# Kernel tuning notes

Measured on AMD Instinct MI355X. Metric: run time of the kernel, lower is better.

Reference implementation:

```python
import jax, jax.numpy as jnp
import numpy as np

N = 100_000      # nodes
E = 1_600_000    # edges (avg degree 16)
IN_DIM = 256
HID = 128
N_OUT = 2


def _linear_params(key, fan_in, fan_out):
    kw, kb = jax.random.split(key)
    bound = 1.0 / np.sqrt(fan_in)
    W = jax.random.uniform(kw, (fan_in, fan_out), jnp.float32, -bound, bound)
    b = jax.random.uniform(kb, (fan_out,), jnp.float32, -bound, bound)
    return W, b


def setup_inputs() -> dict:
    key = jax.random.key(0)
    ks = jax.random.split(key, 6)
    edge_index = jax.random.randint(ks[0], (2, E), 0, N, dtype=jnp.int64)
    x = jax.random.normal(ks[1], (N, IN_DIM), jnp.float32)
    Wi, bi = _linear_params(ks[2], IN_DIM, HID)   # NodeInitializer.lin
    W1, b1 = _linear_params(ks[3], HID, HID)      # GCNConv 1
    W2, b2 = _linear_params(ks[4], HID, HID)      # GCNConv 2
    Wh, bh = _linear_params(ks[5], HID, N_OUT)    # head
    return {"edge_index": edge_index, "x": x, "Wi": Wi, "bi": bi,
            "W1": W1, "b1": b1, "W2": W2, "b2": b2, "Wh": Wh, "bh": bh}


def reference(edge_index, x, Wi, bi, W1, b1, W2, b2, Wh, bh):
    n = x.shape[0]
    # GCNConv preprocessing: add self-loops, symmetric degree normalization.
    loops = jnp.arange(n, dtype=edge_index.dtype)
    src = jnp.concatenate([edge_index[0], loops])  # message source
    dst = jnp.concatenate([edge_index[1], loops])  # aggregation target
    deg = jax.ops.segment_sum(jnp.ones(src.shape[0], jnp.float32), dst, num_segments=n)
    dinv = jnp.where(deg > 0, deg ** -0.5, 0.0)
    norm = dinv[src] * dinv[dst]                   # [E+N]

    # NodeInitializer: relu(linear(x)); dropout = identity (eval mode)
    h = jax.nn.relu(x @ Wi + bi)

    # Two GCNConv layers (no relu between, matching SimpleGCN.forward)
    for W, b in ((W1, b1), (W2, b2)):
        msg = (h @ W)[src] * norm[:, None]         # gather + normalize, [E+N, HID]
        h = jax.ops.segment_sum(msg, dst, num_segments=n) + b  # scatter-add

    return h @ Wh + bh                             # [N, N_OUT]
```

## Files before the change

### kernel.cpp

```cpp
#include <hip/hip_runtime.h>
#include <hip/hip_bf16.h>

#define N_NODES 100000
#define N_EDGES 1600000
#define DIM_IN  256
#define DIM_H   128

#define NBKT 782
#define CPAD 16
#define CAP  4096
#define EPB  8192
#define NBLK ((N_EDGES + EPB - 1) / EPB)

typedef __attribute__((ext_vector_type(8))) short short8;
typedef __attribute__((ext_vector_type(4))) float f32x4;

__device__ __forceinline__ int get_src(const int* e, int is64, int i) {
  return is64 ? e[2 * i] : e[i];
}
__device__ __forceinline__ int get_dst(const int* e, int is64, int i) {
  return is64 ? e[2 * (N_EDGES + i)] : e[N_EDGES + i];
}

__device__ __forceinline__ ushort f2bf(float f) {
  unsigned u = __float_as_uint(f);
  unsigned r = (u + 0x7fffu + ((u >> 16) & 1u)) >> 16;
  return (ushort)r;
}
__device__ __forceinline__ float bf2f(ushort h) {
  return __uint_as_float(((unsigned)h) << 16);
}

__device__ __forceinline__ void load8(const float* p, float* o) {
  float4 a = reinterpret_cast<const float4*>(p)[0];
  float4 b = reinterpret_cast<const float4*>(p)[1];
  o[0] = a.x; o[1] = a.y; o[2] = a.z; o[3] = a.w;
  o[4] = b.x; o[5] = b.y; o[6] = b.z; o[7] = b.w;
}

__device__ __forceinline__ void cvt_split(const float* v, short8& h, short8& l) {
#pragma unroll
  for (int j = 0; j < 8; ++j) {
    ushort hb = f2bf(v[j]);
    ushort lb = f2bf(v[j] - bf2f(hb));
    h[j] = (short)hb;
    l[j] = (short)lb;
  }
}

__global__ __launch_bounds__(256)
void k_prep(const float* __restrict__ Wi, const float* __restrict__ W1,
            const float* __restrict__ W2, const float* __restrict__ Wh,
            const float* __restrict__ b1, const float* __restrict__ b2,
            const float* __restrict__ bh, ushort* __restrict__ outHi,
            float* __restrict__ Wcc, int* __restrict__ bcnt) {
  __shared__ float Wc2s[DIM_H][2];
  constexpr int CH = DIM_IN / 32;
  if (blockIdx.x == 17) {
    for (int i = threadIdx.x; i < NBKT * CPAD; i += 256) bcnt[i] = 0;
    return;
  }
  if (blockIdx.x == 16) {
    const int t = threadIdx.x;
    const int i = t >> 1, j = t & 1;
    float s = 0.f;
#pragma unroll 4
    for (int m = 0; m < DIM_H; ++m) s += W2[(size_t)i * DIM_H + m] * Wh[m * 2 + j];
    Wc2s[i][j] = s;
    __syncthreads();
    float c = 0.f;
#pragma unroll 4
    for (int k = 0; k < DIM_H; ++k) c += W1[(size_t)i * DIM_H + k] * Wc2s[k][j];
    Wcc[i * 2 + j] = c;
    if (t < 2) {
      float a = 0.f, b = 0.f;
      for (int k = 0; k < DIM_H; ++k) {
        a += b1[k] * Wc2s[k][t];
        b += b2[k] * Wh[k * 2 + t];
      }
      Wcc[256 + t] = a;
      Wcc[258 + t] = b + bh[t];
    }
    return;
  }
  int idx = blockIdx.x * 256 + threadIdx.x;
  int n  = idx & 15;
  int qq = (idx >> 4) & 3;
  int nt = (idx >> 6) & 7;
  int c  = idx >> 9;
  int col = nt * 16 + n;
  short8 h8, l8;
#pragma unroll
  for (int j = 0; j < 8; ++j) {
    float v = Wi[(size_t)(c * 32 + qq * 8 + j) * DIM_H + col];
    ushort hb = f2bf(v);
    ushort lb = f2bf(v - bf2f(hb));
    h8[j] = (short)hb;
    l8[j] = (short)lb;
  }
  ((short8*)outHi)[idx] = h8;
  ((short8*)outHi)[CH * 512 + idx] = l8;
}

__global__ __launch_bounds__(1024)
void k_bin1(const int* __restrict__ eidx, int* __restrict__ bcnt,
            unsigned* __restrict__ ebuf) {
  __shared__ int hist[NBKT];
  __shared__ int curL[NBKT];
  __shared__ int s_or;
  const int t = threadIdx.x;
  if (t == 0) s_or = 0;
  for (int i = t; i < NBKT; i += 1024) hist[i] = 0;
  __syncthreads();
  if (eidx[2 * t + 1] != 0) atomicOr(&s_or, 1);
  __syncthreads();
  const int is64 = (s_or == 0);

  unsigned rec[EPB / 1024];
  int bkt[EPB / 1024];
#pragma unroll
  for (int j = 0; j < EPB / 1024; ++j) {
    int e = blockIdx.x * EPB + j * 1024 + t;
    bkt[j] = -1;
    rec[j] = 0;
    if (e < N_EDGES) {
      unsigned s = (unsigned)get_src(eidx, is64, e);
      unsigned d = (unsigned)get_dst(eidx, is64, e);
      if (s < N_NODES && d < N_NODES) {
        bkt[j] = (int)(d >> 7);
        rec[j] = s | ((d & 127u) << 17);
        atomicAdd(&hist[bkt[j]], 1);
      }
    }
  }
  __syncthreads();
  for (int i = t; i < NBKT; i += 1024) {
    int h = hist[i];
    curL[i] = h ? atomicAdd(&bcnt[i * CPAD], h) : 0;
  }
  __syncthreads();
#pragma unroll
  for (int j = 0; j < EPB / 1024; ++j) {
    if (bkt[j] >= 0) {
      int pos = atomicAdd(&curL[bkt[j]], 1);
      ebuf[(size_t)bkt[j] * CAP + pos] = rec[j];
    }
  }
}

__global__ __launch_bounds__(256)
void k_dinvB(const int* __restrict__ bcnt, const unsigned* __restrict__ ebuf,
             float* __restrict__ dinv) {
  __shared__ int hist[128];
  const int b = blockIdx.x, t = threadIdx.x;
  if (t < 128) hist[t] = 0;
  __syncthreads();
  const int cnt = bcnt[b * CPAD];
  const unsigned* eb = ebuf + (size_t)b * CAP;
  for (int i = t; i < cnt; i += 256) atomicAdd(&hist[eb[i] >> 17], 1);
  __syncthreads();
  if (t < 128) {
    int node = (b << 7) + t;
    if (node < N_NODES) dinv[node] = rsqrtf(1.0f + (float)hist[t]);
  }
}

template <int K>
__global__ __launch_bounds__(256, 4)
void k_gemm_xz(const float* __restrict__ A, const ushort* __restrict__ Bfrag,
               const float* __restrict__ bias, const float* __restrict__ Wcc,
               const float* __restrict__ dinv, float4* __restrict__ tbl) {
  constexpr int CH = K / 32;
  __shared__ __align__(16) ushort AhiS[2][256 * 8];
  __shared__ __align__(16) ushort AloS[2][256 * 8];
  const int tid = threadIdx.x;
  const int m0 = blockIdx.x * 64;
  const int wave = tid >> 6, lane = tid & 63;
  const int m_l = lane & 15, quad = lane >> 4;
  const int rs = tid >> 2, q = tid & 3;

  f32x4 acc[2][4];
#pragma unroll
  for (int i = 0; i < 2; ++i)
#pragma unroll
    for (int j = 0; j < 4; ++j) acc[i][j] = (f32x4){0.f, 0.f, 0.f, 0.f};

  const short8* Bhi8 = (const short8*)Bfrag;
  const short8* Blo8 = Bhi8 + CH * 512;
  short8* Ah = (short8*)AhiS;
  short8* Al = (short8*)AloS;

  const int gr = m0 + rs;
  const float* Ap = &A[(size_t)((gr < N_NODES) ? gr : (N_NODES - 1)) * K + q * 8];
  const int went = (rs >> 4) * 64 + q * 16 + ((rs & 15) ^ (q << 2));
  const int rent = quad * 16 + (m_l ^ (quad << 2));

  {
    float v[8];
    load8(Ap, v);
    short8 h, l;
    cvt_split(v, h, l);
    Ah[went] = h;
    Al[went] = l;
  }
  const int bq = quad * 16 + m_l;
  short8 bh0 = Bhi8[(wave * 2 + 0) * 64 + bq];
  short8 bl0 = Blo8[(wave * 2 + 0) * 64 + bq];
  short8 bh1 = Bhi8[(wave * 2 + 1) * 64 + bq];
  short8 bl1 = Blo8[(wave * 2 + 1) * 64 + bq];
  __syncthreads();

#pragma unroll
  for (int c = 0; c < CH; ++c) {
    const int cur = c & 1, nxt = cur ^ 1;
    float vn[8];
    short8 nbh0, nbl0, nbh1, nbl1;
    if (c + 1 < CH) {
      load8(Ap + (c + 1) * 32, vn);
      const int b0 = ((c + 1) * 8 + wave * 2 + 0) * 64 + bq;
      const int b1 = ((c + 1) * 8 + wave * 2 + 1) * 64 + bq;
      nbh0 = Bhi8[b0]; nbl0 = Blo8[b0];
      nbh1 = Bhi8[b1]; nbl1 = Blo8[b1];
    }
    const short8* AhC = Ah + cur * 256;
    const short8* AlC = Al + cur * 256;
#pragma unroll
    for (int mt = 0; mt < 4; ++mt) {
      short8 ahi = AhC[mt * 64 + rent];
      short8 alo = AlC[mt * 64 + rent];
      acc[0][mt] = __builtin_amdgcn_mfma_f32_16x16x32_bf16(ahi, bh0, acc[0][mt], 0, 0, 0);
      acc[0][mt] = __builtin_amdgcn_mfma_f32_16x16x32_bf16(ahi, bl0, acc[0][mt], 0, 0, 0);
      acc[0][mt] = __builtin_amdgcn_mfma_f32_16x16x32_bf16(alo, bh0, acc[0][mt], 0, 0, 0);
      acc[1][mt] = __builtin_amdgcn_mfma_f32_16x16x32_bf16(ahi, bh1, acc[1][mt], 0, 0, 0);
      acc[1][mt] = __builtin_amdgcn_mfma_f32_16x16x32_bf16(ahi, bl1, acc[1][mt], 0, 0, 0);
      acc[1][mt] = __builtin_amdgcn_mfma_f32_16x16x32_bf16(alo, bh1, acc[1][mt], 0, 0, 0);
    }
    if (c + 1 < CH) {
      short8 h, l;
      cvt_split(vn, h, l);
      Ah[nxt * 256 + went] = h;
      Al[nxt * 256 + went] = l;
      bh0 = nbh0; bl0 = nbl0; bh1 = nbh1; bl1 = nbl1;
    }
    __syncthreads();
  }

  float p0[4][4], p1[4][4];
#pragma unroll
  for (int mt = 0; mt < 4; ++mt)
#pragma unroll
    for (int r = 0; r < 4; ++r) { p0[mt][r] = 0.f; p1[mt][r] = 0.f; }
#pragma unroll
  for (int ntl = 0; ntl < 2; ++ntl) {
    const int colg = (wave * 2 + ntl) * 16 + m_l;
    const float bv = bias[colg];
    const float w0 = Wcc[colg * 2 + 0];
    const float w1 = Wcc[colg * 2 + 1];
#pragma unroll
    for (int mt = 0; mt < 4; ++mt)
#pragma unroll
      for (int r = 0; r < 4; ++r) {
        float hv = fmaxf(acc[ntl][mt][r] + bv, 0.f);
        p0[mt][r] += hv * w0;
        p1[mt][r] += hv * w1;
      }
  }
#pragma unroll
  for (int o = 1; o < 16; o <<= 1) {
#pragma unroll
    for (int mt = 0; mt < 4; ++mt)
#pragma unroll
      for (int r = 0; r < 4; ++r) {
        p0[mt][r] += __shfl_xor(p0[mt][r], o);
        p1[mt][r] += __shfl_xor(p1[mt][r], o);
      }
  }
  float* zred = (float*)AhiS;
  if (m_l == 0) {
#pragma unroll
    for (int mt = 0; mt < 4; ++mt)
#pragma unroll
      for (int r = 0; r < 4; ++r) {
        zred[(((0 * 4 + wave) * 4 + quad) * 4 + mt) * 4 + r] = p0[mt][r];
        zred[(((1 * 4 + wave) * 4 + quad) * 4 + mt) * 4 + r] = p1[mt][r];
      }
  }
  __syncthreads();
  if (tid < 64) {
    const int mt = tid >> 4, qd = (tid >> 2) & 3, r = tid & 3;
    const int rowg = m0 + tid;
    if (rowg < N_NODES) {
      float s0 = 0.f, s1 = 0.f;
#pragma unroll
      for (int w = 0; w < 4; ++w) {
        s0 += zred[(((0 * 4 + w) * 4 + qd) * 4 + mt) * 4 + r];
        s1 += zred[(((1 * 4 + w) * 4 + qd) * 4 + mt) * 4 + r];
      }
      float dn = dinv[rowg];
      tbl[rowg] = make_float4(dn * s0, dn * s1, dn, 0.f);
    }
  }
}

__global__ __launch_bounds__(256)
void k_aggr1B(const int* __restrict__ bcnt, const unsigned* __restrict__ ebuf,
              const float4* __restrict__ tbl, float2* __restrict__ tb2,
              float* __restrict__ g) {
  __shared__ float acc[128][4];
  const int b = blockIdx.x, t = threadIdx.x;
  if (t < 128) { acc[t][0] = 0.f; acc[t][1] = 0.f; acc[t][2] = 0.f; }
  __syncthreads();
  const int cnt = bcnt[b * CPAD];
  const unsigned* eb = ebuf + (size_t)b * CAP;
  for (int i = t; i < cnt; i += 256) {
    unsigned r = eb[i];
    float4 v = tbl[r & 0x1FFFFu];
    int d = r >> 17;
    atomicAdd(&acc[d][0], v.x);
    atomicAdd(&acc[d][1], v.y);
    atomicAdd(&acc[d][2], v.z);
  }
  __syncthreads();
  if (t < 128) {
    int node = (b << 7) + t;
    if (node < N_NODES) {
      float4 self = tbl[node];
      float dn = self.z;
      tb2[node] = make_float2(dn * dn * (acc[t][0] + self.x),
                              dn * dn * (acc[t][1] + self.y));
      g[node] = dn * (acc[t][2] + self.z);
    }
  }
}

__global__ __launch_bounds__(256)
void k_aggr2B(const int* __restrict__ bcnt, const unsigned* __restrict__ ebuf,
              const float2* __restrict__ tb2, const float4* __restrict__ tbl,
              const float* __restrict__ g, const float* __restrict__ tail,
              float* __restrict__ out) {
  __shared__ float acc[128][2];
  const int b = blockIdx.x, t = threadIdx.x;
  if (t < 128) { acc[t][0] = 0.f; acc[t][1] = 0.f; }
  __syncthreads();
  const int cnt = bcnt[b * CPAD];
  const unsigned* eb = ebuf + (size_t)b * CAP;
  for (int i = t; i < cnt; i += 256) {
    unsigned r = eb[i];
    float2 v = tb2[r & 0x1FFFFu];
    int d = r >> 17;
    atomicAdd(&acc[d][0], v.x);
    atomicAdd(&acc[d][1], v.y);
  }
  __syncthreads();
  if (t < 128) {
    int node = (b << 7) + t;
    if (node < N_NODES) {
      float2 self = tb2[node];
      float dn = tbl[node].z;
      float gv = g[node];
      float o0 = dn * (acc[t][0] + self.x) + gv * tail[0] + tail[2];
      float o1 = dn * (acc[t][1] + self.y) + gv * tail[1] + tail[3];
      reinterpret_cast<float2*>(out)[node] = make_float2(o0, o1);
    }
  }
}

__global__ __launch_bounds__(1024) void k_detect(const int* __restrict__ e,
                                                 int* __restrict__ flag) {
  __shared__ int s;
  if (threadIdx.x == 0) s = 0;
  __syncthreads();
  atomicOr(&s, e[2 * threadIdx.x + 1]);
  __syncthreads();
  if (threadIdx.x == 0) *flag = (s == 0) ? 1 : 0;
}

__global__ __launch_bounds__(256) void k_zero(int* __restrict__ p, int n) {
  int i = blockIdx.x * 256 + threadIdx.x;
  if (i < n) p[i] = 0;
}

__global__ __launch_bounds__(256) void k_count(const int* __restrict__ eidx,
                                               const int* __restrict__ flag,
                                               int* __restrict__ off) {
  int e = blockIdx.x * 256 + threadIdx.x;
  int is64 = *flag;
  if (e < N_EDGES) {
    unsigned d = (unsigned)get_dst(eidx, is64, e);
    if (d < N_NODES) atomicAdd(&off[d], 1);
  }
}

__global__ __launch_bounds__(256) void k_dinv_old(const int* __restrict__ off,
                                                  float* __restrict__ dinv) {
  int i = blockIdx.x * 256 + threadIdx.x;
  if (i < N_NODES) dinv[i] = rsqrtf(1.0f + (float)off[i]);
}

template <int K>
__global__ __launch_bounds__(256)
void k_gemm(const float* __restrict__ A, const float* __restrict__ B,
            const float* __restrict__ bias, const float* __restrict__ scale,
            float* __restrict__ C, const int do_relu) {
  __shared__ float As[64][33];
  const int tid = threadIdx.x;
  const int tx = tid & 15;
  const int ty = tid >> 4;
  const int m0 = blockIdx.x * 64;

  float acc[4][8];
#pragma unroll
  for (int i = 0; i < 4; ++i)
#pragma unroll
    for (int j = 0; j < 8; ++j) acc[i][j] = 0.f;

  const int rs = tid >> 2;
  const int ks = (tid & 3) * 8;

  for (int k0 = 0; k0 < K; k0 += 32) {
    float av8[8];
    const int gm = m0 + rs;
    if (gm < N_NODES) {
      load8(&A[(size_t)gm * K + k0 + ks], av8);
    } else {
#pragma unroll
      for (int j = 0; j < 8; ++j) av8[j] = 0.f;
    }
    __syncthreads();
#pragma unroll
    for (int j = 0; j < 8; ++j) As[rs][ks + j] = av8[j];
    __syncthreads();

    const float* Bp = B + (size_t)k0 * DIM_H + tx * 8;
#pragma unroll 4
    for (int k = 0; k < 32; ++k) {
      float bv[8];
      load8(Bp + (size_t)k * DIM_H, bv);
      float av[4];
#pragma unroll
      for (int rr = 0; rr < 4; ++rr) av[rr] = As[ty * 4 + rr][k];
#pragma unroll
      for (int rr = 0; rr < 4; ++rr)
#pragma unroll
        for (int cc = 0; cc < 8; ++cc)
          acc[rr][cc] = fmaf(av[rr], bv[cc], acc[rr][cc]);
    }
  }

  float bs[8];
  if (bias) {
    load8(bias + tx * 8, bs);
  } else {
#pragma unroll
    for (int j = 0; j < 8; ++j) bs[j] = 0.f;
  }
#pragma unroll
  for (int rr = 0; rr < 4; ++rr) {
    const int gm = m0 + ty * 4 + rr;
    if (gm < N_NODES) {
      float sc = scale ? scale[gm] : 1.0f;
      float v[8];
#pragma unroll
      for (int cc = 0; cc < 8; ++cc) {
        float t = acc[rr][cc] + bs[cc];
        if (do_relu) t = fmaxf(t, 0.f);
        v[cc] = t * sc;
      }
      float* Cp = &C[(size_t)gm * DIM_H + tx * 8];
      reinterpret_cast<float4*>(Cp)[0] = make_float4(v[0], v[1], v[2], v[3]);
      reinterpret_cast<float4*>(Cp)[1] = make_float4(v[4], v[5], v[6], v[7]);
    }
  }
}

__global__ __launch_bounds__(256)
void k_aggr_init(const float* __restrict__ t, const float* __restrict__ dinv,
                 const float* __restrict__ bias, float* __restrict__ h) {
  int idx = blockIdx.x * 256 + threadIdx.x;
  if (idx < N_NODES * DIM_H) {
    int i = idx >> 7;
    int c = idx & 127;
    float d = dinv[i];
    h[idx] = bias[c] + t[idx] * d * d;
  }
}

__global__ __launch_bounds__(256)
void k_aggr_edges(const int* __restrict__ eidx, const int* __restrict__ flag,
                  const float* __restrict__ t, const float* __restrict__ dinv,
                  float* __restrict__ h) {
  int e = blockIdx.x * 2 + (threadIdx.x >> 7);
  int c = threadIdx.x & 127;
  int is64 = *flag;
  if (e < N_EDGES) {
    unsigned s = (unsigned)get_src(eidx, is64, e);
    unsigned d = (unsigned)get_dst(eidx, is64, e);
    if (s < N_NODES && d < N_NODES) {
      float nrm = dinv[s] * dinv[d];
      unsafeAtomicAdd(&h[(size_t)d * DIM_H + c], t[(size_t)s * DIM_H + c] * nrm);
    }
  }
}

__global__ __launch_bounds__(256)
void k_head_f32(const float* __restrict__ h, const float* __restrict__ Wh,
                const float* __restrict__ bh, float* __restrict__ out) {
  int node = blockIdx.x * 4 + (threadIdx.x >> 6);
  int lane = threadIdx.x & 63;
  if (node >= N_NODES) return;
  float h0 = h[(size_t)node * DIM_H + lane];
  float h1 = h[(size_t)node * DIM_H + 64 + lane];
  float s0 = h0 * Wh[lane * 2 + 0] + h1 * Wh[(lane + 64) * 2 + 0];
  float s1 = h0 * Wh[lane * 2 + 1] + h1 * Wh[(lane + 64) * 2 + 1];
#pragma unroll
  for (int off = 32; off > 0; off >>= 1) {
    s0 += __shfl_down(s0, off);
    s1 += __shfl_down(s1, off);
  }
  if (lane == 0) {
    reinterpret_cast<float2*>(out)[node] = make_float2(s0 + bh[0], s1 + bh[1]);
  }
}

extern "C" void kernel_launch(void* const* d_in, const int* in_sizes, int n_in,
                              void* d_out, int out_size, void* d_ws, size_t ws_size,
                              hipStream_t stream) {
  (void)in_sizes; (void)n_in; (void)out_size;
  const int* eidx = (const int*)d_in[0];
  const float* x  = (const float*)d_in[1];
  const float* Wi = (const float*)d_in[2];
  const float* bi = (const float*)d_in[3];
  const float* W1 = (const float*)d_in[4];
  const float* b1 = (const float*)d_in[5];
  const float* W2 = (const float*)d_in[6];
  const float* b2 = (const float*)d_in[7];
  const float* Wh = (const float*)d_in[8];
  const float* bh = (const float*)d_in[9];
  float* out = (float*)d_out;

  const int gE  = (N_EDGES + 255) / 256;
  const int gM  = (N_NODES + 63) / 64;
  const int gW  = (N_NODES + 3) / 4;

  char* ws = (char*)d_ws;

  const size_t need1 = 16201600;

  if (ws_size >= need1) {
    float*    Wcc  = (float*)(ws + 4096);
    ushort*   bfWi = (ushort*)(ws + 8192);
    int*      bcnt = (int*)(ws + 139264);
    float*    dinv = (float*)(ws + 189312);
    float4*   tbl  = (float4*)(ws + 589312);
    float2*   tb2  = (float2*)(ws + 2189312);
    float*    g    = (float*)(ws + 2989312);
    unsigned* ebuf = (unsigned*)(ws + 3389312);

    k_prep<<<18, 256, 0, stream>>>(Wi, W1, W2, Wh, b1, b2, bh, bfWi, Wcc, bcnt);
    k_bin1<<<NBLK, 1024, 0, stream>>>(eidx, bcnt, ebuf);
    k_dinvB<<<NBKT, 256, 0, stream>>>(bcnt, ebuf, dinv);
    k_gemm_xz<DIM_IN><<<gM, 256, 0, stream>>>(x, bfWi, bi, Wcc, dinv, tbl);
    k_aggr1B<<<NBKT, 256, 0, stream>>>(bcnt, ebuf, tbl, tb2, g);
    k_aggr2B<<<NBKT, 256, 0, stream>>>(bcnt, ebuf, tb2, tbl, g, Wcc + 256, out);
  } else {
    const int gN  = (N_NODES + 255) / 256;
    int*   flag = (int*)ws;
    int*   off  = (int*)(ws + 4096);
    float* dinv = (float*)(ws + 404480);
    float* fbA  = (float*)(ws + 804864);
    float* fbB  = (float*)(ws + 804864 + (size_t)N_NODES * DIM_H * 4);
    const int gNH = (N_NODES * DIM_H + 255) / 256;
    const int gE2 = (N_EDGES + 1) / 2;
    k_detect<<<1, 1024, 0, stream>>>(eidx, flag);
    k_zero<<<gN, 256, 0, stream>>>(off, N_NODES);
    k_count<<<gE, 256, 0, stream>>>(eidx, flag, off);
    k_dinv_old<<<gN, 256, 0, stream>>>(off, dinv);

    k_gemm<DIM_IN><<<gM, 256, 0, stream>>>(x, Wi, bi, nullptr, fbA, 1);
    k_gemm<DIM_H><<<gM, 256, 0, stream>>>(fbA, W1, nullptr, nullptr, fbB, 0);
    k_aggr_init<<<gNH, 256, 0, stream>>>(fbB, dinv, b1, fbA);
    k_aggr_edges<<<gE2, 256, 0, stream>>>(eidx, flag, fbB, dinv, fbA);
    k_gemm<DIM_H><<<gM, 256, 0, stream>>>(fbA, W2, nullptr, nullptr, fbB, 0);
    k_aggr_init<<<gNH, 256, 0, stream>>>(fbB, dinv, b2, fbA);
    k_aggr_edges<<<gE2, 256, 0, stream>>>(eidx, flag, fbB, dinv, fbA);
    k_head_f32<<<gW, 256, 0, stream>>>(fbA, Wh, bh, out);
  }
}
```

Baseline: 291.2 us.

## Stage whole A tile in LDS upfront and reduce epilogue via padded LDS

The GEMM kernel now loads the entire 64xK fp32 A tile at the start with contiguous coalesced loads. It converts the tile to bf16 hi/lo and stores it in LDS, replacing the per-chunk double-buffered loads and per-chunk barriers. The epilogue's shuffle-based 16-lane reduction is replaced by writes to a padded LDS array that 64 threads sum serially. LDS use grows (about 64KB for K=256), so launch bounds drop to 2 blocks per CU, and the serial 64-term reduction on one wave may cost time.

```diff
diff --git a/kernel.cpp b/kernel.cpp
--- a/kernel.cpp
+++ b/kernel.cpp
@@ -166,42 +166,38 @@
 }
 
 template <int K>
-__global__ __launch_bounds__(256, 4)
+__global__ __launch_bounds__(256, 2)
 void k_gemm_xz(const float* __restrict__ A, const ushort* __restrict__ Bfrag,
                const float* __restrict__ bias, const float* __restrict__ Wcc,
                const float* __restrict__ dinv, float4* __restrict__ tbl) {
   constexpr int CH = K / 32;
-  __shared__ __align__(16) ushort AhiS[2][256 * 8];
-  __shared__ __align__(16) ushort AloS[2][256 * 8];
+  __shared__ __align__(16) ushort AS[2 * CH * 256 * 8];
   const int tid = threadIdx.x;
   const int m0 = blockIdx.x * 64;
   const int wave = tid >> 6, lane = tid & 63;
   const int m_l = lane & 15, quad = lane >> 4;
-  const int rs = tid >> 2, q = tid & 3;
-
-  f32x4 acc[2][4];
-#pragma unroll
-  for (int i = 0; i < 2; ++i)
-#pragma unroll
-    for (int j = 0; j < 4; ++j) acc[i][j] = (f32x4){0.f, 0.f, 0.f, 0.f};
 
   const short8* Bhi8 = (const short8*)Bfrag;
   const short8* Blo8 = Bhi8 + CH * 512;
-  short8* Ah = (short8*)AhiS;
-  short8* Al = (short8*)AloS;
-
-  const int gr = m0 + rs;
-  const float* Ap = &A[(size_t)((gr < N_NODES) ? gr : (N_NODES - 1)) * K + q * 8];
-  const int went = (rs >> 4) * 64 + q * 16 + ((rs & 15) ^ (q << 2));
-  const int rent = quad * 16 + (m_l ^ (quad << 2));
-
-  {
+  short8* A8 = (short8*)AS;
+
+  const size_t xlim = (size_t)N_NODES * K * 4 - 32;
+  const size_t gbase = (size_t)m0 * K * 4;
+#pragma unroll
+  for (int rr = 0; rr < 8; ++rr) {
+    const size_t off = (size_t)rr * 8192 + (size_t)tid * 32;
+    size_t ga = gbase + off;
+    if (ga > xlim) ga = xlim;
     float v[8];
-    load8(Ap, v);
+    load8((const float*)((const char*)A + ga), v);
     short8 h, l;
     cvt_split(v, h, l);
-    Ah[went] = h;
-    Al[went] = l;
+    const int row = (int)(off >> 10);
+    const int byr = (int)(off & 1023);
+    const int c = byr >> 7, q = (byr >> 5) & 3;
+    const int ent = c * 256 + (row >> 4) * 64 + q * 16 + ((row & 15) ^ (q << 2));
+    A8[ent] = h;
+    A8[2048 + ent] = l;
   }
   const int bq = quad * 16 + m_l;
   short8 bh0 = Bhi8[(wave * 2 + 0) * 64 + bq];
@@ -210,20 +206,24 @@
   short8 bl1 = Blo8[(wave * 2 + 1) * 64 + bq];
   __syncthreads();
 
+  f32x4 acc[2][4];
+#pragma unroll
+  for (int i = 0; i < 2; ++i)
+#pragma unroll
+    for (int j = 0; j < 4; ++j) acc[i][j] = (f32x4){0.f, 0.f, 0.f, 0.f};
+
+  const int rent = quad * 16 + (m_l ^ (quad << 2));
 #pragma unroll
   for (int c = 0; c < CH; ++c) {
-    const int cur = c & 1, nxt = cur ^ 1;
-    float vn[8];
     short8 nbh0, nbl0, nbh1, nbl1;
     if (c + 1 < CH) {
-      load8(Ap + (c + 1) * 32, vn);
       const int b0 = ((c + 1) * 8 + wave * 2 + 0) * 64 + bq;
       const int b1 = ((c + 1) * 8 + wave * 2 + 1) * 64 + bq;
       nbh0 = Bhi8[b0]; nbl0 = Blo8[b0];
       nbh1 = Bhi8[b1]; nbl1 = Blo8[b1];
     }
-    const short8* AhC = Ah + cur * 256;
-    const short8* AlC = Al + cur * 256;
+    const short8* AhC = A8 + c * 256;
+    const short8* AlC = A8 + 2048 + c * 256;
 #pragma unroll
     for (int mt = 0; mt < 4; ++mt) {
       short8 ahi = AhC[mt * 64 + rent];
@@ -236,13 +236,8 @@
       acc[1][mt] = __builtin_amdgcn_mfma_f32_16x16x32_bf16(alo, bh1, acc[1][mt], 0, 0, 0);
     }
     if (c + 1 < CH) {
-      short8 h, l;
-      cvt_split(vn, h, l);
-      Ah[nxt * 256 + went] = h;
-      Al[nxt * 256 + went] = l;
       bh0 = nbh0; bl0 = nbl0; bh1 = nbh1; bl1 = nbl1;
     }
-    __syncthreads();
   }
 
   float p0[4][4], p1[4][4];
@@ -265,37 +260,34 @@
         p1[mt][r] += hv * w1;
       }
   }
-#pragma unroll
-  for (int o = 1; o < 16; o <<= 1) {
+  __syncthreads();
+  float* zs = (float*)AS;
+  {
+    const int base = ((wave * 4 + quad) * 16 + m_l) * 33;
 #pragma unroll
     for (int mt = 0; mt < 4; ++mt)
 #pragma unroll
       for (int r = 0; r < 4; ++r) {
-        p0[mt][r] += __shfl_xor(p0[mt][r], o);
-        p1[mt][r] += __shfl_xor(p1[mt][r], o);
+        zs[base + mt * 4 + r]      = p0[mt][r];
+        zs[base + 16 + mt * 4 + r] = p1[mt][r];
       }
   }
-  float* zred = (float*)AhiS;
-  if (m_l == 0) {
-#pragma unroll
-    for (int mt = 0; mt < 4; ++mt)
-#pragma unroll
-      for (int r = 0; r < 4; ++r) {
-        zred[(((0 * 4 + wave) * 4 + quad) * 4 + mt) * 4 + r] = p0[mt][r];
-        zred[(((1 * 4 + wave) * 4 + quad) * 4 + mt) * 4 + r] = p1[mt][r];
+  __syncthreads();
+  if (tid < 64) {
+    const int row = tid;
+    const int mt = row >> 4, qd = (row >> 2) & 3, r = row & 3;
+    float s0 = 0.f, s1 = 0.f;
+#pragma unroll
+    for (int w = 0; w < 4; ++w) {
+      const int wb = (w * 4 + qd) * 16 * 33;
+#pragma unroll
+      for (int ml = 0; ml < 16; ++ml) {
+        s0 += zs[wb + ml * 33 + mt * 4 + r];
+        s1 += zs[wb + ml * 33 + 16 + mt * 4 + r];
       }
-  }
-  __syncthreads();
-  if (tid < 64) {
-    const int mt = tid >> 4, qd = (tid >> 2) & 3, r = tid & 3;
-    const int rowg = m0 + tid;
+    }
+    const int rowg = m0 + row;
     if (rowg < N_NODES) {
-      float s0 = 0.f, s1 = 0.f;
-#pragma unroll
-      for (int w = 0; w < 4; ++w) {
-        s0 += zred[(((0 * 4 + w) * 4 + qd) * 4 + mt) * 4 + r];
-        s1 += zred[(((1 * 4 + w) * 4 + qd) * 4 + mt) * 4 + r];
-      }
       float dn = dinv[rowg];
       tbl[rowg] = make_float4(dn * s0, dn * s1, dn, 0.f);
     }
```

Result: no change. 292.3 us (+0.4%).

## Fuse edge binning with input GEMM in one launch and compute degree via global atomics

Applied to the files above, without the earlier changes.

Merges the edge-bucketing kernel and the feature GEMM into a single heterogeneous launch, where the first blocks bin edges and the rest run the GEMM. The goal is to let the memory-bound binning overlap with the compute-heavy GEMM and to drop a launch boundary. Degrees are now counted with global atomics during binning instead of in a separate histogram pass, and a small scale kernel afterwards applies dinv. This adds contention from per-edge global atomics, an extra ztmp round trip, and binning blocks shrunk to 256 threads.

```diff
diff --git a/kernel.cpp b/kernel.cpp
--- a/kernel.cpp
+++ b/kernel.cpp
@@ -9,8 +9,9 @@
 #define NBKT 782
 #define CPAD 16
 #define CAP  4096
-#define EPB  8192
-#define NBLK ((N_EDGES + EPB - 1) / EPB)
+#define EPB2 4096
+#define NBLK2 ((N_EDGES + EPB2 - 1) / EPB2)
+#define GEMM_BLKS ((N_NODES + 63) / 64)
 
 typedef __attribute__((ext_vector_type(8))) short short8;
 typedef __attribute__((ext_vector_type(4))) float f32x4;
@@ -53,9 +54,15 @@
             const float* __restrict__ W2, const float* __restrict__ Wh,
             const float* __restrict__ b1, const float* __restrict__ b2,
             const float* __restrict__ bh, ushort* __restrict__ outHi,
-            float* __restrict__ Wcc, int* __restrict__ bcnt) {
+            float* __restrict__ Wcc, int* __restrict__ bcnt,
+            int* __restrict__ deg) {
   __shared__ float Wc2s[DIM_H][2];
   constexpr int CH = DIM_IN / 32;
+  if (blockIdx.x >= 18) {
+    int i = (blockIdx.x - 18) * 256 + threadIdx.x;
+    if (i < N_NODES) deg[i] = 0;
+    return;
+  }
   if (blockIdx.x == 17) {
     for (int i = threadIdx.x; i < NBKT * CPAD; i += 256) bcnt[i] = 0;
     return;
@@ -102,79 +109,62 @@
   ((short8*)outHi)[CH * 512 + idx] = l8;
 }
 
-__global__ __launch_bounds__(1024)
-void k_bin1(const int* __restrict__ eidx, int* __restrict__ bcnt,
-            unsigned* __restrict__ ebuf) {
-  __shared__ int hist[NBKT];
-  __shared__ int curL[NBKT];
-  __shared__ int s_or;
-  const int t = threadIdx.x;
-  if (t == 0) s_or = 0;
-  for (int i = t; i < NBKT; i += 1024) hist[i] = 0;
-  __syncthreads();
-  if (eidx[2 * t + 1] != 0) atomicOr(&s_or, 1);
-  __syncthreads();
-  const int is64 = (s_or == 0);
-
-  unsigned rec[EPB / 1024];
-  int bkt[EPB / 1024];
-#pragma unroll
-  for (int j = 0; j < EPB / 1024; ++j) {
-    int e = blockIdx.x * EPB + j * 1024 + t;
-    bkt[j] = -1;
-    rec[j] = 0;
-    if (e < N_EDGES) {
-      unsigned s = (unsigned)get_src(eidx, is64, e);
-      unsigned d = (unsigned)get_dst(eidx, is64, e);
-      if (s < N_NODES && d < N_NODES) {
-        bkt[j] = (int)(d >> 7);
-        rec[j] = s | ((d & 127u) << 17);
-        atomicAdd(&hist[bkt[j]], 1);
-      }
-    }
-  }
-  __syncthreads();
-  for (int i = t; i < NBKT; i += 1024) {
-    int h = hist[i];
-    curL[i] = h ? atomicAdd(&bcnt[i * CPAD], h) : 0;
-  }
-  __syncthreads();
-#pragma unroll
-  for (int j = 0; j < EPB / 1024; ++j) {
-    if (bkt[j] >= 0) {
-      int pos = atomicAdd(&curL[bkt[j]], 1);
-      ebuf[(size_t)bkt[j] * CAP + pos] = rec[j];
-    }
-  }
-}
-
-__global__ __launch_bounds__(256)
-void k_dinvB(const int* __restrict__ bcnt, const unsigned* __restrict__ ebuf,
-             float* __restrict__ dinv) {
-  __shared__ int hist[128];
-  const int b = blockIdx.x, t = threadIdx.x;
-  if (t < 128) hist[t] = 0;
-  __syncthreads();
-  const int cnt = bcnt[b * CPAD];
-  const unsigned* eb = ebuf + (size_t)b * CAP;
-  for (int i = t; i < cnt; i += 256) atomicAdd(&hist[eb[i] >> 17], 1);
-  __syncthreads();
-  if (t < 128) {
-    int node = (b << 7) + t;
-    if (node < N_NODES) dinv[node] = rsqrtf(1.0f + (float)hist[t]);
-  }
-}
-
-template <int K>
 __global__ __launch_bounds__(256, 4)
-void k_gemm_xz(const float* __restrict__ A, const ushort* __restrict__ Bfrag,
-               const float* __restrict__ bias, const float* __restrict__ Wcc,
-               const float* __restrict__ dinv, float4* __restrict__ tbl) {
-  constexpr int CH = K / 32;
-  __shared__ __align__(16) ushort AhiS[2][256 * 8];
-  __shared__ __align__(16) ushort AloS[2][256 * 8];
+void k_main(const int* __restrict__ eidx, const float* __restrict__ A,
+            const ushort* __restrict__ Bfrag, const float* __restrict__ bias,
+            const float* __restrict__ Wcc, int* __restrict__ bcnt,
+            unsigned* __restrict__ ebuf, int* __restrict__ deg,
+            float2* __restrict__ ztmp) {
+  __shared__ __align__(16) char smem[16384];
   const int tid = threadIdx.x;
-  const int m0 = blockIdx.x * 64;
+
+  if (blockIdx.x < NBLK2) {
+    int* hist = (int*)smem;
+    int* curL = hist + NBKT;
+    int* sorp = curL + NBKT;
+    if (tid == 0) *sorp = 0;
+    for (int i = tid; i < NBKT; i += 256) hist[i] = 0;
+    __syncthreads();
+    if (eidx[2 * tid + 1] != 0) atomicOr(sorp, 1);
+    __syncthreads();
+    const int is64 = (*sorp == 0);
+
+    unsigned rec[16];
+    int bkt[16];
+#pragma unroll
+    for (int j = 0; j < 16; ++j) {
+      int e = blockIdx.x * EPB2 + j * 256 + tid;
+      bkt[j] = -1;
+      rec[j] = 0;
+      if (e < N_EDGES) {
+        unsigned s = (unsigned)get_src(eidx, is64, e);
+        unsigned d = (unsigned)get_dst(eidx, is64, e);
+        if (s < N_NODES && d < N_NODES) {
+          bkt[j] = (int)(d >> 7);
+          rec[j] = s | ((d & 127u) << 17);
+          atomicAdd(&hist[bkt[j]], 1);
+          atomicAdd(&deg[d], 1);
+        }
+      }
+    }
+    __syncthreads();
+    for (int i = tid; i < NBKT; i += 256) {
+      int h = hist[i];
+      curL[i] = h ? atomicAdd(&bcnt[i * CPAD], h) : 0;
+    }
+    __syncthreads();
+#pragma unroll
+    for (int j = 0; j < 16; ++j) {
+      if (bkt[j] >= 0) {
+        int pos = atomicAdd(&curL[bkt[j]], 1);
+        ebuf[(size_t)bkt[j] * CAP + pos] = rec[j];
+      }
+    }
+    return;
+  }
+
+  constexpr int CH = DIM_IN / 32;
+  const int m0 = (blockIdx.x - NBLK2) * 64;
   const int wave = tid >> 6, lane = tid & 63;
   const int m_l = lane & 15, quad = lane >> 4;
   const int rs = tid >> 2, q = tid & 3;
@@ -187,11 +177,11 @@
 
   const short8* Bhi8 = (const short8*)Bfrag;
   const short8* Blo8 = Bhi8 + CH * 512;
-  short8* Ah = (short8*)AhiS;
-  short8* Al = (short8*)AloS;
+  short8* Ah = (short8*)smem;
+  short8* Al = (short8*)(smem + 8192);
 
   const int gr = m0 + rs;
-  const float* Ap = &A[(size_t)((gr < N_NODES) ? gr : (N_NODES - 1)) * K + q * 8];
+  const float* Ap = &A[(size_t)((gr < N_NODES) ? gr : (N_NODES - 1)) * DIM_IN + q * 8];
   const int went = (rs >> 4) * 64 + q * 16 + ((rs & 15) ^ (q << 2));
   const int rent = quad * 16 + (m_l ^ (quad << 2));
 
@@ -275,7 +265,7 @@
         p1[mt][r] += __shfl_xor(p1[mt][r], o);
       }
   }
-  float* zred = (float*)AhiS;
+  float* zred = (float*)smem;
   if (m_l == 0) {
 #pragma unroll
     for (int mt = 0; mt < 4; ++mt)
@@ -296,9 +286,19 @@
         s0 += zred[(((0 * 4 + w) * 4 + qd) * 4 + mt) * 4 + r];
         s1 += zred[(((1 * 4 + w) * 4 + qd) * 4 + mt) * 4 + r];
       }
-      float dn = dinv[rowg];
-      tbl[rowg] = make_float4(dn * s0, dn * s1, dn, 0.f);
-    }
+      ztmp[rowg] = make_float2(s0, s1);
+    }
+  }
+}
+
+__global__ __launch_bounds__(256)
+void k_scale(const int* __restrict__ deg, const float2* __restrict__ ztmp,
+             float4* __restrict__ tbl) {
+  int n = blockIdx.x * 256 + threadIdx.x;
+  if (n < N_NODES) {
+    float dn = rsqrtf(1.0f + (float)deg[n]);
+    float2 z = ztmp[n];
+    tbl[n] = make_float4(dn * z.x, dn * z.y, dn, 0.f);
   }
 }
 
@@ -541,25 +541,28 @@
   const int gE  = (N_EDGES + 255) / 256;
   const int gM  = (N_NODES + 63) / 64;
   const int gW  = (N_NODES + 3) / 4;
+  const int gN256 = (N_NODES + 255) / 256;
 
   char* ws = (char*)d_ws;
 
-  const size_t need1 = 16201600;
+  const size_t need1 = 17001600;
 
   if (ws_size >= need1) {
     float*    Wcc  = (float*)(ws + 4096);
     ushort*   bfWi = (ushort*)(ws + 8192);
     int*      bcnt = (int*)(ws + 139264);
-    float*    dinv = (float*)(ws + 189312);
-    float4*   tbl  = (float4*)(ws + 589312);
-    float2*   tb2  = (float2*)(ws + 2189312);
-    float*    g    = (float*)(ws + 2989312);
-    unsigned* ebuf = (unsigned*)(ws + 3389312);
-
-    k_prep<<<18, 256, 0, stream>>>(Wi, W1, W2, Wh, b1, b2, bh, bfWi, Wcc, bcnt);
-    k_bin1<<<NBLK, 1024, 0, stream>>>(eidx, bcnt, ebuf);
-    k_dinvB<<<NBKT, 256, 0, stream>>>(bcnt, ebuf, dinv);
-    k_gemm_xz<DIM_IN><<<gM, 256, 0, stream>>>(x, bfWi, bi, Wcc, dinv, tbl);
+    int*      deg  = (int*)(ws + 189312);
+    float2*   ztmp = (float2*)(ws + 589312);
+    float4*   tbl  = (float4*)(ws + 1389312);
+    float2*   tb2  = (float2*)(ws + 2989312);
+    float*    g    = (float*)(ws + 3789312);
+    unsigned* ebuf = (unsigned*)(ws + 4189312);
+
+    k_prep<<<18 + gN256, 256, 0, stream>>>(Wi, W1, W2, Wh, b1, b2, bh,
+                                           bfWi, Wcc, bcnt, deg);
+    k_main<<<NBLK2 + GEMM_BLKS, 256, 0, stream>>>(eidx, x, bfWi, bi, Wcc,
+                                                  bcnt, ebuf, deg, ztmp);
+    k_scale<<<gN256, 256, 0, stream>>>(deg, ztmp, tbl);
     k_aggr1B<<<NBKT, 256, 0, stream>>>(bcnt, ebuf, tbl, tb2, g);
     k_aggr2B<<<NBKT, 256, 0, stream>>>(bcnt, ebuf, tb2, tbl, g, Wcc + 256, out);
   } else {
```

New measurement: 319.2 us. +9.6%, slower.
